# Optimization experiments

Hardware: AMD Instinct MI355X
Metric: run time of the kernel (lower is better)

## Reference

```python
import jax, jax.numpy as jnp
import numpy as np

WS = 8        # window_size
NH = 16       # num_heads

def setup_inputs() -> dict:
    key = jax.random.key(0)
    k1, k2, k3, k4 = jax.random.split(key, 4)
    B, N, C = 16, 4096, 512
    x = jax.random.normal(k1, (B, N, C), dtype=jnp.float32)
    w_qkv = jax.random.normal(k2, (3 * C, C), dtype=jnp.float32) * 0.02
    w_proj = jax.random.normal(k3, (C, C), dtype=jnp.float32) * 0.02
    b_proj = jax.random.normal(k4, (C,), dtype=jnp.float32) * 0.02
    return {"x": x, "w_qkv": w_qkv, "w_proj": w_proj, "b_proj": b_proj}

def reference(x, w_qkv, w_proj, b_proj):
    B, N, C = x.shape
    H = W = int(N ** 0.5)
    ws, nh = WS, NH
    hd = C // nh
    scale = hd ** (-0.5)
    winH, winW = H // ws, W // ws

    # --- window partition, faithfully replicating torch unfold+view semantics ---
    # unfold(1).unfold(2).contiguous() memory layout: (B, winH, winW, C, ws_h, ws_w)
    xw = x.reshape(B, winH, ws, winW, ws, C)
    xw = jnp.transpose(xw, (0, 1, 3, 5, 2, 4))  # (B,winH,winW,C,ws,ws) contiguous order
    # torch .view(B,winH,winW,ws,ws,C): pure reshape of that layout (scrambles C/spatial)
    xw = xw.reshape(B, winH, winW, ws, ws, C)
    xw = jnp.transpose(xw, (0, 1, 2, 4, 3, 5)).reshape(-1, ws * ws, C)  # (nW, ws*ws, C)

    # --- qkv projection and per-window attention ---
    qkv = (xw @ w_qkv.T).reshape(-1, ws * ws, 3, nh, hd)
    qkv = jnp.transpose(qkv, (2, 0, 3, 1, 4))  # (3, nW, nh, ws*ws, hd)
    q, k, v = qkv[0], qkv[1], qkv[2]
    attn = jnp.einsum('whid,whjd->whij', q, k) * scale
    attn = jax.nn.softmax(attn, axis=-1)
    o = jnp.einsum('whij,whjd->whid', attn, v)          # (nW, nh, ws*ws, hd)
    o = jnp.transpose(o, (0, 2, 1, 3)).reshape(-1, ws * ws, C)

    o = o @ w_proj.T + b_proj

    # --- window merge (standard permute, as in torch code) ---
    o = o.reshape(B, winH, winW, ws, ws, C)
    o = jnp.transpose(o, (0, 1, 3, 2, 4, 5)).reshape(B, H, W, C)
    return o.reshape(B, N, C)
```

## Files before the change

### kernel.cpp

```cpp
#include <hip/hip_runtime.h>


typedef short s16x8 __attribute__((ext_vector_type(8)));
typedef float f32x4 __attribute__((ext_vector_type(4)));

union V8 { uint4 u4; uint2 u2[2]; s16x8 h; ushort s[8]; uint u[4]; };

__device__ __forceinline__ ushort f2b(float f) {
    union { float f; uint u; } v; v.f = f;
    return (ushort)((v.u + 0x7fffu + ((v.u >> 16) & 1u)) >> 16);
}
__device__ __forceinline__ void cvt8(const float* __restrict__ p, V8& d) {
    union { float4 f; uint u[4]; } a, b;
    a.f = *(const float4*)p;  b.f = *(const float4*)(p + 4);
    d.u[0] = __builtin_amdgcn_perm(a.u[1], a.u[0], 0x07060302u);
    d.u[1] = __builtin_amdgcn_perm(a.u[3], a.u[2], 0x07060302u);
    d.u[2] = __builtin_amdgcn_perm(b.u[1], b.u[0], 0x07060302u);
    d.u[3] = __builtin_amdgcn_perm(b.u[3], b.u[2], 0x07060302u);
}
__device__ __forceinline__ f32x4 mfma16(s16x8 a, s16x8 b, f32x4 c) {
    return __builtin_amdgcn_mfma_f32_16x16x32_bf16(a, b, c, 0, 0, 0);
}
__device__ __forceinline__ uint2 pack4(float a, float b, float c, float d) {
    uint2 r;
    r.x = (uint)f2b(a) | ((uint)f2b(b) << 16);
    r.y = (uint)f2b(c) | ((uint)f2b(d) << 16);
    return r;
}

__global__ __launch_bounds__(256)
void pack_w(const float* __restrict__ wqkv, const float* __restrict__ wproj,
            ushort* __restrict__ dst)
{
    const int gid = blockIdx.x * 256 + threadIdx.x;
    const int o = gid << 3;
    const int colw = (o >> 3) & 15, quad = (o >> 7) & 3, kk = (o >> 9) & 15;
    const int tile = o >> 13;
    const float* src;
    if (o < 786432) {
        const int mat = tile >> 5, nt = tile & 31;
        src = wqkv + (size_t)(mat * 512 + nt * 16 + colw) * 512 + (kk << 5) + (quad << 3);
    } else {
        const int nt = tile - 96;
        src = wproj + (size_t)(nt * 16 + colw) * 512 + (kk << 5) + (quad << 3);
    }
    float4 a = *(const float4*)src, b = *(const float4*)(src + 4);
    V8 v;
    v.s[0] = f2b(a.x); v.s[1] = f2b(a.y); v.s[2] = f2b(a.z); v.s[3] = f2b(a.w);
    v.s[4] = f2b(b.x); v.s[5] = f2b(b.y); v.s[6] = f2b(b.z); v.s[7] = f2b(b.w);
    *(uint4*)(dst + o) = v.u4;
}

template<bool PK>
__global__ __launch_bounds__(1024, 4)
void win_fused(const float* __restrict__ x, const void* __restrict__ Wq,
               const void* __restrict__ Wp, const float* __restrict__ bproj,
               float* __restrict__ out)
{
    __shared__ __align__(16) ushort xw[32768];
    __shared__ __align__(16) ushort scr[32768];

    char* const sb = (char*)scr;
    const int tid  = threadIdx.x;
    const int lane = tid & 63;
    const int wave = tid >> 6;
    const int col  = lane & 15, quad = lane >> 4;
    const int win  = blockIdx.x;
    const int bb = win >> 6, wh = (win >> 3) & 7, ww = win & 7;
    const size_t xbase = (size_t)(bb * 4096) * 512;

    {
        const int m8 = lane;
        const int u8 = wave & 7;
        const int dh = wave >> 3;
        const int t  = ((m8 & 7) << 3) | (m8 >> 3);
        const int ch0 = m8 << 3;
        const float* gp = x + xbase
            + (size_t)(wh * 512 + u8 * 64 + ww * 8 + dh * 4) * 512 + ch0;
        V8 L[4];
        #pragma unroll
        for (int i = 0; i < 4; ++i) cvt8(gp + i * 512, L[i]);
        #pragma unroll
        for (int e = 0; e < 8; ++e) {
            union { uint2 u; ushort s[4]; } Wv;
            #pragma unroll
            for (int i = 0; i < 4; ++i) Wv.s[i] = L[i].s[e];
            const int c8 = (e << 3) | u8;
            *(uint2*)(&xw[(t << 9) + ((c8 ^ (t & 7)) << 3) + (dh << 2)]) = Wv.u;
        }
    }
    __syncthreads();

    const int hhg = wave >> 2;
    const int mh  = (wave >> 1) & 1;
    const int nhf = wave & 1;
    const int tw  = wave & 3;

    f32x4 pacc[4][2];
    #pragma unroll
    for (int mt = 0; mt < 4; ++mt) {
        pacc[mt][0] = (f32x4){0.f, 0.f, 0.f, 0.f};
        pacc[mt][1] = (f32x4){0.f, 0.f, 0.f, 0.f};
    }

    for (int p = 0; p < 4; ++p) {
        const int h = (p << 2) | hhg;

        f32x4 c00 = {0.f,0.f,0.f,0.f}, c01 = {0.f,0.f,0.f,0.f}, c02 = {0.f,0.f,0.f,0.f};
        f32x4 c10 = {0.f,0.f,0.f,0.f}, c11 = {0.f,0.f,0.f,0.f}, c12 = {0.f,0.f,0.f,0.f};
        size_t wb0 = 0, wb1 = 0, wb2 = 0;
        const float *f0 = nullptr, *f1 = nullptr, *f2 = nullptr;
        if constexpr (PK) {
            if (nhf == 0) { wb0 = (size_t)(2*h)   * 8192; wb1 = (size_t)(2*h+1)  * 8192;
                            wb2 = (size_t)(32+2*h)* 8192; }
            else          { wb0 = (size_t)(32+2*h+1)*8192; wb1 = (size_t)(64+2*h)*8192;
                            wb2 = (size_t)(64+2*h+1)*8192; }
        } else {
            const float* W = (const float*)Wq;
            if (nhf == 0) {
                f0 = W + (size_t)(h*32 + col) * 512;
                f1 = W + (size_t)(h*32 + 16 + col) * 512;
                f2 = W + (size_t)(512 + h*32 + col) * 512;
            } else {
                f0 = W + (size_t)(512 + h*32 + 16 + col) * 512;
                f1 = W + (size_t)(1024 + h*32 + col) * 512;
                f2 = W + (size_t)(1024 + h*32 + 16 + col) * 512;
            }
        }
        #pragma unroll 2
        for (int kk = 0; kk < 16; ++kk) {
            const int c8 = (kk << 2) | quad;
            V8 a0, a1;
            { const int t = mh*32 + col;      a0.u4 = *(const uint4*)(&xw[(t << 9) + ((c8 ^ (t & 7)) << 3)]); }
            { const int t = mh*32 + 16 + col; a1.u4 = *(const uint4*)(&xw[(t << 9) + ((c8 ^ (t & 7)) << 3)]); }
            V8 b0, b1, b2;
            if constexpr (PK) {
                const ushort* W = (const ushort*)Wq;
                const int lo = (kk << 9) + (lane << 3);
                b0.u4 = *(const uint4*)(&W[wb0 + lo]);
                b1.u4 = *(const uint4*)(&W[wb1 + lo]);
                b2.u4 = *(const uint4*)(&W[wb2 + lo]);
            } else {
                cvt8(f0 + (kk << 5) + (quad << 3), b0);
                cvt8(f1 + (kk << 5) + (quad << 3), b1);
                cvt8(f2 + (kk << 5) + (quad << 3), b2);
            }
            c00 = mfma16(a0.h, b0.h, c00);
            c01 = mfma16(a0.h, b1.h, c01);
            c02 = mfma16(a0.h, b2.h, c02);
            c10 = mfma16(a1.h, b0.h, c10);
            c11 = mfma16(a1.h, b1.h, c11);
            c12 = mfma16(a1.h, b2.h, c12);
        }

        {
            const int hb = hhg * 12288;
            #pragma unroll
            for (int mt = 0; mt < 2; ++mt) {
                const int tokb = mh*32 + mt*16 + (quad << 2);
                const f32x4& d0 = mt ? c10 : c00;
                const f32x4& d1 = mt ? c11 : c01;
                const f32x4& d2 = mt ? c12 : c02;
                if (nhf == 0) {
                    #pragma unroll
                    for (int r = 0; r < 4; ++r) {
                        const int rowb = hb + ((tokb + r) << 6);
                        *(ushort*)(sb + rowb + ((col*2)      ^ (quad << 4))) = f2b(d0[r]);
                        *(ushort*)(sb + rowb + ((32 + col*2) ^ (quad << 4))) = f2b(d1[r]);
                        *(ushort*)(sb + 4096 + rowb + ((col*2) ^ (quad << 4))) = f2b(d2[r]);
                    }
                } else {
                    #pragma unroll
                    for (int r = 0; r < 4; ++r) {
                        const int rowb = hb + ((tokb + r) << 6);
                        *(ushort*)(sb + 4096 + rowb + ((32 + col*2) ^ (quad << 4))) = f2b(d0[r]);
                    }
                    const int tsw = (tokb * 2) ^ ((col & 7) << 4);
                    *(uint2*)(sb + hb + 8192 + col * 128 + tsw) =
                        pack4(d1[0], d1[1], d1[2], d1[3]);
                    *(uint2*)(sb + hb + 8192 + (16 + col) * 128 + tsw) =
                        pack4(d2[0], d2[1], d2[2], d2[3]);
                }
            }
        }
        __syncthreads();

        const int ab = hhg * 12288;
        const int sr = ((col >> 2) & 3) << 4;
        V8 kf0, kf1, kf2, kf3, qf;
        kf0.u4 = *(const uint4*)(sb + ab + 4096 + ((0*16 + col) << 6) + ((quad << 4) ^ sr));
        kf1.u4 = *(const uint4*)(sb + ab + 4096 + ((1*16 + col) << 6) + ((quad << 4) ^ sr));
        kf2.u4 = *(const uint4*)(sb + ab + 4096 + ((2*16 + col) << 6) + ((quad << 4) ^ sr));
        kf3.u4 = *(const uint4*)(sb + ab + 4096 + ((3*16 + col) << 6) + ((quad << 4) ^ sr));
        qf.u4  = *(const uint4*)(sb + ab + (((tw << 4) + col) << 6) + ((quad << 4) ^ sr));
        f32x4 ST[4];
        ST[0] = mfma16(kf0.h, qf.h, (f32x4){0.f,0.f,0.f,0.f});
        ST[1] = mfma16(kf1.h, qf.h, (f32x4){0.f,0.f,0.f,0.f});
        ST[2] = mfma16(kf2.h, qf.h, (f32x4){0.f,0.f,0.f,0.f});
        ST[3] = mfma16(kf3.h, qf.h, (f32x4){0.f,0.f,0.f,0.f});

        const float smul = 0.17677669529663689f * 1.4426950408889634f;
        float m0 = ST[0][0];
        #pragma unroll
        for (int a = 0; a < 4; ++a)
            #pragma unroll
            for (int r = 0; r < 4; ++r) m0 = fmaxf(m0, ST[a][r]);
        m0 = fmaxf(m0, __shfl_xor(m0, 16));
        m0 = fmaxf(m0, __shfl_xor(m0, 32));
        float s0 = 0.f;
        #pragma unroll
        for (int a = 0; a < 4; ++a)
            #pragma unroll
            for (int r = 0; r < 4; ++r) {
                const float pv = exp2f((ST[a][r] - m0) * smul);
                ST[a][r] = pv; s0 += pv;
            }
        s0 += __shfl_xor(s0, 16);
        s0 += __shfl_xor(s0, 32);
        const float inv = 1.0f / s0;

        const uint2 pk0 = pack4(ST[0][0], ST[0][1], ST[0][2], ST[0][3]);
        const uint2 pk1 = pack4(ST[1][0], ST[1][1], ST[1][2], ST[1][3]);
        const uint2 pk2 = pack4(ST[2][0], ST[2][1], ST[2][2], ST[2][3]);
        const uint2 pk3 = pack4(ST[3][0], ST[3][1], ST[3][2], ST[3][3]);
        const int srcA = ((quad & 1) << 5) + col;
        const int srcB = srcA + 16;
        const bool hi = quad >= 2;
        f32x4 OT0 = {0.f,0.f,0.f,0.f}, OT1 = {0.f,0.f,0.f,0.f};
        const int vsw = (col & 7) << 4;
        {
            const uint a0x = __shfl((int)pk0.x, srcA), a0y = __shfl((int)pk0.y, srcA);
            const uint b0x = __shfl((int)pk0.x, srcB), b0y = __shfl((int)pk0.y, srcB);
            const uint a1x = __shfl((int)pk1.x, srcA), a1y = __shfl((int)pk1.y, srcA);
            const uint b1x = __shfl((int)pk1.x, srcB), b1y = __shfl((int)pk1.y, srcB);
            V8 pf;
            pf.u[0] = hi ? a1x : a0x;  pf.u[1] = hi ? a1y : a0y;
            pf.u[2] = hi ? b1x : b0x;  pf.u[3] = hi ? b1y : b0y;
            V8 vf0, vf1;
            vf0.u4 = *(const uint4*)(sb + ab + 8192 + ((0*16 + col) << 7) + (((quad << 4)) ^ vsw));
            vf1.u4 = *(const uint4*)(sb + ab + 8192 + ((16 + col) << 7)   + (((quad << 4)) ^ vsw));
            OT0 = mfma16(vf0.h, pf.h, OT0);
            OT1 = mfma16(vf1.h, pf.h, OT1);
        }
        {
            const uint a0x = __shfl((int)pk2.x, srcA), a0y = __shfl((int)pk2.y, srcA);
            const uint b0x = __shfl((int)pk2.x, srcB), b0y = __shfl((int)pk2.y, srcB);
            const uint a1x = __shfl((int)pk3.x, srcA), a1y = __shfl((int)pk3.y, srcA);
            const uint b1x = __shfl((int)pk3.x, srcB), b1y = __shfl((int)pk3.y, srcB);
            V8 pf;
            pf.u[0] = hi ? a1x : a0x;  pf.u[1] = hi ? a1y : a0y;
            pf.u[2] = hi ? b1x : b0x;  pf.u[3] = hi ? b1y : b0y;
            V8 vf0, vf1;
            vf0.u4 = *(const uint4*)(sb + ab + 8192 + ((0*16 + col) << 7) + ((64 + (quad << 4)) ^ vsw));
            vf1.u4 = *(const uint4*)(sb + ab + 8192 + ((16 + col) << 7)   + ((64 + (quad << 4)) ^ vsw));
            OT0 = mfma16(vf0.h, pf.h, OT0);
            OT1 = mfma16(vf1.h, pf.h, OT1);
        }

        {
            const int rowb = 49152 + (((tw << 4) + col) << 8);
            const int osw = (col & 3) << 5;
            const int ch2a = hhg*64 + (quad << 3);
            *(uint2*)(sb + rowb + (ch2a ^ osw)) =
                pack4(OT0[0]*inv, OT0[1]*inv, OT0[2]*inv, OT0[3]*inv);
            *(uint2*)(sb + rowb + ((ch2a + 32) ^ osw)) =
                pack4(OT1[0]*inv, OT1[1]*inv, OT1[2]*inv, OT1[3]*inv);
        }
        __syncthreads();

        #pragma unroll 2
        for (int kkl = 0; kkl < 4; ++kkl) {
            const int kkg = (p << 2) | kkl;
            V8 a0, a1, a2, a3;
            const int cb = ((kkl << 6) + (quad << 4));
            const int osw = (col & 3) << 5;
            a0.u4 = *(const uint4*)(sb + 49152 + ((0*16 + col) << 8) + (cb ^ osw));
            a1.u4 = *(const uint4*)(sb + 49152 + ((1*16 + col) << 8) + (cb ^ osw));
            a2.u4 = *(const uint4*)(sb + 49152 + ((2*16 + col) << 8) + (cb ^ osw));
            a3.u4 = *(const uint4*)(sb + 49152 + ((3*16 + col) << 8) + (cb ^ osw));
            #pragma unroll
            for (int nt = 0; nt < 2; ++nt) {
                s16x8 b;
                if constexpr (PK) {
                    const ushort* W = (const ushort*)Wp;
                    V8 v; v.u4 = *(const uint4*)(&W[(size_t)(((wave*2 + nt)*16) + kkg) * 512
                                                    + (lane << 3)]);
                    b = v.h;
                } else {
                    const float* W = (const float*)Wp;
                    V8 v; cvt8(W + (size_t)(wave*32 + nt*16 + col) * 512
                                 + (kkg << 5) + (quad << 3), v);
                    b = v.h;
                }
                pacc[0][nt] = mfma16(a0.h, b, pacc[0][nt]);
                pacc[1][nt] = mfma16(a1.h, b, pacc[1][nt]);
                pacc[2][nt] = mfma16(a2.h, b, pacc[2][nt]);
                pacc[3][nt] = mfma16(a3.h, b, pacc[3][nt]);
            }
        }
    }

    const size_t wbase = (size_t)(bb * 4096 + wh * 512 + ww * 8) * 512;
    const float bv0 = bproj[wave*32 + col];
    const float bv1 = bproj[wave*32 + 16 + col];
    #pragma unroll
    for (int mt = 0; mt < 4; ++mt)
        #pragma unroll
        for (int r = 0; r < 4; ++r) {
            const int t = (mt << 4) + (quad << 2) + r;
            float* op = out + wbase + (size_t)(((t >> 3) << 6) + (t & 7)) * 512
                        + wave*32;
            op[col]      = pacc[mt][0][r] + bv0;
            op[16 + col] = pacc[mt][1][r] + bv1;
        }
}

extern "C" void kernel_launch(void* const* d_in, const int* in_sizes, int n_in,
                              void* d_out, int out_size, void* d_ws, size_t ws_size,
                              hipStream_t stream) {
    const float* x     = (const float*)d_in[0];
    const float* wqkv  = (const float*)d_in[1];
    const float* wproj = (const float*)d_in[2];
    const float* bproj = (const float*)d_in[3];
    float* out = (float*)d_out;
    (void)in_sizes; (void)n_in; (void)out_size;

    if (ws_size >= 2097152) {
        ushort* wpk = (ushort*)d_ws;
        pack_w<<<dim3(512), dim3(256), 0, stream>>>(wqkv, wproj, wpk);
        win_fused<true><<<dim3(1024), dim3(1024), 0, stream>>>(
            x, wpk, wpk + 786432, bproj, out);
    } else {
        win_fused<false><<<dim3(1024), dim3(1024), 0, stream>>>(
            x, wqkv, wproj, bproj, out);
    }
}
```

Before: 428.4 us.

## Process eight heads per pass with full-token QKV tiles per wave

Each wave now computes QKV for one head across all 64 tokens, so 8 heads are handled per pass instead of 4. This halves the outer head-group loop from 4 passes to 2 and each weight fragment load is reused across four M tiles instead of two, which cuts redundant weight traffic. Shared memory is enlarged to one 160KB buffer so the scratch area can hold eight heads. Attention then handles two query tiles per wave, and the projection runs over eight K-steps per pass. In exchange there are more accumulator registers and more LDS, which may limit occupancy.

```diff
diff --git a/kernel.cpp b/kernel.cpp
--- a/kernel.cpp
+++ b/kernel.cpp
@@ -57,10 +57,10 @@
                const void* __restrict__ Wp, const float* __restrict__ bproj,
                float* __restrict__ out)
 {
-    __shared__ __align__(16) ushort xw[32768];
-    __shared__ __align__(16) ushort scr[32768];
-
-    char* const sb = (char*)scr;
+    __shared__ __align__(16) ushort sm[81920];
+    ushort* const xw = sm;
+    char* const sb = (char*)(sm + 32768);
+
     const int tid  = threadIdx.x;
     const int lane = tid & 63;
     const int wave = tid >> 6;
@@ -91,10 +91,8 @@
     }
     __syncthreads();
 
-    const int hhg = wave >> 2;
-    const int mh  = (wave >> 1) & 1;
-    const int nhf = wave & 1;
-    const int tw  = wave & 3;
+    const int hh  = wave >> 1;
+    const int tri = wave & 1;
 
     f32x4 pacc[4][2];
     #pragma unroll
@@ -102,22 +100,26 @@
         pacc[mt][0] = (f32x4){0.f, 0.f, 0.f, 0.f};
         pacc[mt][1] = (f32x4){0.f, 0.f, 0.f, 0.f};
     }
-
-    for (int p = 0; p < 4; ++p) {
-        const int h = (p << 2) | hhg;
-
-        f32x4 c00 = {0.f,0.f,0.f,0.f}, c01 = {0.f,0.f,0.f,0.f}, c02 = {0.f,0.f,0.f,0.f};
-        f32x4 c10 = {0.f,0.f,0.f,0.f}, c11 = {0.f,0.f,0.f,0.f}, c12 = {0.f,0.f,0.f,0.f};
+    const float smul = 0.17677669529663689f * 1.4426950408889634f;
+
+    for (int p = 0; p < 2; ++p) {
+        const int h = (p << 3) | hh;
+
+        f32x4 c[4][3];
+        #pragma unroll
+        for (int mt = 0; mt < 4; ++mt)
+            #pragma unroll
+            for (int nt = 0; nt < 3; ++nt) c[mt][nt] = (f32x4){0.f, 0.f, 0.f, 0.f};
         size_t wb0 = 0, wb1 = 0, wb2 = 0;
         const float *f0 = nullptr, *f1 = nullptr, *f2 = nullptr;
         if constexpr (PK) {
-            if (nhf == 0) { wb0 = (size_t)(2*h)   * 8192; wb1 = (size_t)(2*h+1)  * 8192;
-                            wb2 = (size_t)(32+2*h)* 8192; }
-            else          { wb0 = (size_t)(32+2*h+1)*8192; wb1 = (size_t)(64+2*h)*8192;
-                            wb2 = (size_t)(64+2*h+1)*8192; }
+            if (tri == 0) { wb0 = (size_t)(2*h)     * 8192; wb1 = (size_t)(2*h+1)  * 8192;
+                            wb2 = (size_t)(32+2*h)  * 8192; }
+            else          { wb0 = (size_t)(32+2*h+1)* 8192; wb1 = (size_t)(64+2*h) * 8192;
+                            wb2 = (size_t)(64+2*h+1)* 8192; }
         } else {
             const float* W = (const float*)Wq;
-            if (nhf == 0) {
+            if (tri == 0) {
                 f0 = W + (size_t)(h*32 + col) * 512;
                 f1 = W + (size_t)(h*32 + 16 + col) * 512;
                 f2 = W + (size_t)(512 + h*32 + col) * 512;
@@ -130,9 +132,6 @@
         #pragma unroll 2
         for (int kk = 0; kk < 16; ++kk) {
             const int c8 = (kk << 2) | quad;
-            V8 a0, a1;
-            { const int t = mh*32 + col;      a0.u4 = *(const uint4*)(&xw[(t << 9) + ((c8 ^ (t & 7)) << 3)]); }
-            { const int t = mh*32 + 16 + col; a1.u4 = *(const uint4*)(&xw[(t << 9) + ((c8 ^ (t & 7)) << 3)]); }
             V8 b0, b1, b2;
             if constexpr (PK) {
                 const ushort* W = (const ushort*)Wq;
@@ -145,157 +144,169 @@
                 cvt8(f1 + (kk << 5) + (quad << 3), b1);
                 cvt8(f2 + (kk << 5) + (quad << 3), b2);
             }
-            c00 = mfma16(a0.h, b0.h, c00);
-            c01 = mfma16(a0.h, b1.h, c01);
-            c02 = mfma16(a0.h, b2.h, c02);
-            c10 = mfma16(a1.h, b0.h, c10);
-            c11 = mfma16(a1.h, b1.h, c11);
-            c12 = mfma16(a1.h, b2.h, c12);
-        }
+            #pragma unroll
+            for (int mt = 0; mt < 4; ++mt) {
+                const int t = (mt << 4) + col;
+                V8 a; a.u4 = *(const uint4*)(&xw[(t << 9) + ((c8 ^ (t & 7)) << 3)]);
+                c[mt][0] = mfma16(a.h, b0.h, c[mt][0]);
+                c[mt][1] = mfma16(a.h, b1.h, c[mt][1]);
+                c[mt][2] = mfma16(a.h, b2.h, c[mt][2]);
+            }
+        }
+
+        if (p) __syncthreads();
 
         {
-            const int hb = hhg * 12288;
-            #pragma unroll
-            for (int mt = 0; mt < 2; ++mt) {
-                const int tokb = mh*32 + mt*16 + (quad << 2);
-                const f32x4& d0 = mt ? c10 : c00;
-                const f32x4& d1 = mt ? c11 : c01;
-                const f32x4& d2 = mt ? c12 : c02;
-                if (nhf == 0) {
+            const int hb = hh * 12288;
+            if (tri == 0) {
+                #pragma unroll
+                for (int mt = 0; mt < 4; ++mt)
                     #pragma unroll
                     for (int r = 0; r < 4; ++r) {
-                        const int rowb = hb + ((tokb + r) << 6);
-                        *(ushort*)(sb + rowb + ((col*2)      ^ (quad << 4))) = f2b(d0[r]);
-                        *(ushort*)(sb + rowb + ((32 + col*2) ^ (quad << 4))) = f2b(d1[r]);
-                        *(ushort*)(sb + 4096 + rowb + ((col*2) ^ (quad << 4))) = f2b(d2[r]);
+                        const int tok  = (mt << 4) + (quad << 2) + r;
+                        const int rowb = hb + (tok << 6);
+                        const int s    = quad << 4;
+                        *(ushort*)(sb + rowb + ((col*2)        ^ s)) = f2b(c[mt][0][r]);
+                        *(ushort*)(sb + rowb + ((32 + col*2)   ^ s)) = f2b(c[mt][1][r]);
+                        *(ushort*)(sb + 4096 + rowb + ((col*2) ^ s)) = f2b(c[mt][2][r]);
                     }
-                } else {
+            } else {
+                #pragma unroll
+                for (int mt = 0; mt < 4; ++mt) {
                     #pragma unroll
                     for (int r = 0; r < 4; ++r) {
-                        const int rowb = hb + ((tokb + r) << 6);
-                        *(ushort*)(sb + 4096 + rowb + ((32 + col*2) ^ (quad << 4))) = f2b(d0[r]);
+                        const int tok = (mt << 4) + (quad << 2) + r;
+                        *(ushort*)(sb + hb + 4096 + (tok << 6)
+                                   + ((32 + col*2) ^ (quad << 4))) = f2b(c[mt][0][r]);
                     }
-                    const int tsw = (tokb * 2) ^ ((col & 7) << 4);
-                    *(uint2*)(sb + hb + 8192 + col * 128 + tsw) =
-                        pack4(d1[0], d1[1], d1[2], d1[3]);
+                    const int tok0 = (mt << 4) + (quad << 2);
+                    const int tsw  = (tok0 * 2) ^ ((col & 7) << 4);
+                    *(uint2*)(sb + hb + 8192 + col * 128        + tsw) =
+                        pack4(c[mt][1][0], c[mt][1][1], c[mt][1][2], c[mt][1][3]);
                     *(uint2*)(sb + hb + 8192 + (16 + col) * 128 + tsw) =
-                        pack4(d2[0], d2[1], d2[2], d2[3]);
+                        pack4(c[mt][2][0], c[mt][2][1], c[mt][2][2], c[mt][2][3]);
                 }
             }
         }
         __syncthreads();
 
-        const int ab = hhg * 12288;
-        const int sr = ((col >> 2) & 3) << 4;
-        V8 kf0, kf1, kf2, kf3, qf;
-        kf0.u4 = *(const uint4*)(sb + ab + 4096 + ((0*16 + col) << 6) + ((quad << 4) ^ sr));
-        kf1.u4 = *(const uint4*)(sb + ab + 4096 + ((1*16 + col) << 6) + ((quad << 4) ^ sr));
-        kf2.u4 = *(const uint4*)(sb + ab + 4096 + ((2*16 + col) << 6) + ((quad << 4) ^ sr));
-        kf3.u4 = *(const uint4*)(sb + ab + 4096 + ((3*16 + col) << 6) + ((quad << 4) ^ sr));
-        qf.u4  = *(const uint4*)(sb + ab + (((tw << 4) + col) << 6) + ((quad << 4) ^ sr));
-        f32x4 ST[4];
-        ST[0] = mfma16(kf0.h, qf.h, (f32x4){0.f,0.f,0.f,0.f});
-        ST[1] = mfma16(kf1.h, qf.h, (f32x4){0.f,0.f,0.f,0.f});
-        ST[2] = mfma16(kf2.h, qf.h, (f32x4){0.f,0.f,0.f,0.f});
-        ST[3] = mfma16(kf3.h, qf.h, (f32x4){0.f,0.f,0.f,0.f});
-
-        const float smul = 0.17677669529663689f * 1.4426950408889634f;
-        float m0 = ST[0][0];
-        #pragma unroll
-        for (int a = 0; a < 4; ++a)
-            #pragma unroll
-            for (int r = 0; r < 4; ++r) m0 = fmaxf(m0, ST[a][r]);
-        m0 = fmaxf(m0, __shfl_xor(m0, 16));
-        m0 = fmaxf(m0, __shfl_xor(m0, 32));
-        float s0 = 0.f;
-        #pragma unroll
-        for (int a = 0; a < 4; ++a)
-            #pragma unroll
-            for (int r = 0; r < 4; ++r) {
-                const float pv = exp2f((ST[a][r] - m0) * smul);
-                ST[a][r] = pv; s0 += pv;
-            }
-        s0 += __shfl_xor(s0, 16);
-        s0 += __shfl_xor(s0, 32);
-        const float inv = 1.0f / s0;
-
-        const uint2 pk0 = pack4(ST[0][0], ST[0][1], ST[0][2], ST[0][3]);
-        const uint2 pk1 = pack4(ST[1][0], ST[1][1], ST[1][2], ST[1][3]);
-        const uint2 pk2 = pack4(ST[2][0], ST[2][1], ST[2][2], ST[2][3]);
-        const uint2 pk3 = pack4(ST[3][0], ST[3][1], ST[3][2], ST[3][3]);
-        const int srcA = ((quad & 1) << 5) + col;
-        const int srcB = srcA + 16;
-        const bool hi = quad >= 2;
-        f32x4 OT0 = {0.f,0.f,0.f,0.f}, OT1 = {0.f,0.f,0.f,0.f};
-        const int vsw = (col & 7) << 4;
         {
-            const uint a0x = __shfl((int)pk0.x, srcA), a0y = __shfl((int)pk0.y, srcA);
-            const uint b0x = __shfl((int)pk0.x, srcB), b0y = __shfl((int)pk0.y, srcB);
-            const uint a1x = __shfl((int)pk1.x, srcA), a1y = __shfl((int)pk1.y, srcA);
-            const uint b1x = __shfl((int)pk1.x, srcB), b1y = __shfl((int)pk1.y, srcB);
-            V8 pf;
-            pf.u[0] = hi ? a1x : a0x;  pf.u[1] = hi ? a1y : a0y;
-            pf.u[2] = hi ? b1x : b0x;  pf.u[3] = hi ? b1y : b0y;
-            V8 vf0, vf1;
-            vf0.u4 = *(const uint4*)(sb + ab + 8192 + ((0*16 + col) << 7) + (((quad << 4)) ^ vsw));
-            vf1.u4 = *(const uint4*)(sb + ab + 8192 + ((16 + col) << 7)   + (((quad << 4)) ^ vsw));
-            OT0 = mfma16(vf0.h, pf.h, OT0);
-            OT1 = mfma16(vf1.h, pf.h, OT1);
-        }
-        {
-            const uint a0x = __shfl((int)pk2.x, srcA), a0y = __shfl((int)pk2.y, srcA);
-            const uint b0x = __shfl((int)pk2.x, srcB), b0y = __shfl((int)pk2.y, srcB);
-            const uint a1x = __shfl((int)pk3.x, srcA), a1y = __shfl((int)pk3.y, srcA);
-            const uint b1x = __shfl((int)pk3.x, srcB), b1y = __shfl((int)pk3.y, srcB);
-            V8 pf;
-            pf.u[0] = hi ? a1x : a0x;  pf.u[1] = hi ? a1y : a0y;
-            pf.u[2] = hi ? b1x : b0x;  pf.u[3] = hi ? b1y : b0y;
-            V8 vf0, vf1;
-            vf0.u4 = *(const uint4*)(sb + ab + 8192 + ((0*16 + col) << 7) + ((64 + (quad << 4)) ^ vsw));
-            vf1.u4 = *(const uint4*)(sb + ab + 8192 + ((16 + col) << 7)   + ((64 + (quad << 4)) ^ vsw));
-            OT0 = mfma16(vf0.h, pf.h, OT0);
-            OT1 = mfma16(vf1.h, pf.h, OT1);
-        }
-
-        {
-            const int rowb = 49152 + (((tw << 4) + col) << 8);
-            const int osw = (col & 3) << 5;
-            const int ch2a = hhg*64 + (quad << 3);
-            *(uint2*)(sb + rowb + (ch2a ^ osw)) =
-                pack4(OT0[0]*inv, OT0[1]*inv, OT0[2]*inv, OT0[3]*inv);
-            *(uint2*)(sb + rowb + ((ch2a + 32) ^ osw)) =
-                pack4(OT1[0]*inv, OT1[1]*inv, OT1[2]*inv, OT1[3]*inv);
+            const int ab = hh * 12288;
+            const int sr = ((col >> 2) & 3) << 4;
+            s16x8 kf[4];
+            #pragma unroll
+            for (int kt = 0; kt < 4; ++kt) {
+                V8 v; v.u4 = *(const uint4*)(sb + ab + 4096
+                              + (((kt << 4) + col) << 6) + ((quad << 4) ^ sr));
+                kf[kt] = v.h;
+            }
+            float inv[2]; uint2 pk[4][2];
+            #pragma unroll
+            for (int qt = 0; qt < 2; ++qt) {
+                V8 qf; qf.u4 = *(const uint4*)(sb + ab
+                               + ((((tri*2 + qt) << 4) + col) << 6) + ((quad << 4) ^ sr));
+                f32x4 ST[4];
+                #pragma unroll
+                for (int kt = 0; kt < 4; ++kt)
+                    ST[kt] = mfma16(kf[kt], qf.h, (f32x4){0.f,0.f,0.f,0.f});
+                float m0 = ST[0][0];
+                #pragma unroll
+                for (int kt = 0; kt < 4; ++kt)
+                    #pragma unroll
+                    for (int r = 0; r < 4; ++r) m0 = fmaxf(m0, ST[kt][r]);
+                m0 = fmaxf(m0, __shfl_xor(m0, 16));
+                m0 = fmaxf(m0, __shfl_xor(m0, 32));
+                float s0 = 0.f;
+                #pragma unroll
+                for (int kt = 0; kt < 4; ++kt)
+                    #pragma unroll
+                    for (int r = 0; r < 4; ++r) {
+                        const float pv = exp2f((ST[kt][r] - m0) * smul);
+                        ST[kt][r] = pv; s0 += pv;
+                    }
+                s0 += __shfl_xor(s0, 16);
+                s0 += __shfl_xor(s0, 32);
+                inv[qt] = 1.0f / s0;
+                #pragma unroll
+                for (int kt = 0; kt < 4; ++kt)
+                    pk[kt][qt] = pack4(ST[kt][0], ST[kt][1], ST[kt][2], ST[kt][3]);
+            }
+
+            f32x4 OT[2][2];
+            #pragma unroll
+            for (int dt = 0; dt < 2; ++dt) {
+                OT[dt][0] = (f32x4){0.f,0.f,0.f,0.f};
+                OT[dt][1] = (f32x4){0.f,0.f,0.f,0.f};
+            }
+            const int srcA = ((quad & 1) << 5) + col;
+            const int srcB = srcA + 16;
+            const bool hi = quad >= 2;
+            const int vsw = (col & 7) << 4;
+            #pragma unroll
+            for (int kh = 0; kh < 2; ++kh) {
+                s16x8 pf[2];
+                #pragma unroll
+                for (int qt = 0; qt < 2; ++qt) {
+                    const uint2 pkA = pk[kh*2][qt], pkB = pk[kh*2+1][qt];
+                    const uint a0x = __shfl((int)pkA.x, srcA), a0y = __shfl((int)pkA.y, srcA);
+                    const uint b0x = __shfl((int)pkA.x, srcB), b0y = __shfl((int)pkA.y, srcB);
+                    const uint a1x = __shfl((int)pkB.x, srcA), a1y = __shfl((int)pkB.y, srcA);
+                    const uint b1x = __shfl((int)pkB.x, srcB), b1y = __shfl((int)pkB.y, srcB);
+                    V8 t;
+                    t.u[0] = hi ? a1x : a0x;  t.u[1] = hi ? a1y : a0y;
+                    t.u[2] = hi ? b1x : b0x;  t.u[3] = hi ? b1y : b0y;
+                    pf[qt] = t.h;
+                }
+                #pragma unroll
+                for (int dt = 0; dt < 2; ++dt) {
+                    V8 vf; vf.u4 = *(const uint4*)(sb + ab + 8192
+                                   + (((dt << 4) + col) << 7)
+                                   + (((kh << 6) + (quad << 4)) ^ vsw));
+                    OT[dt][0] = mfma16(vf.h, pf[0], OT[dt][0]);
+                    OT[dt][1] = mfma16(vf.h, pf[1], OT[dt][1]);
+                }
+            }
+            __syncthreads();
+
+            #pragma unroll
+            for (int dt = 0; dt < 2; ++dt)
+                #pragma unroll
+                for (int qt = 0; qt < 2; ++qt) {
+                    const int tok   = ((tri*2 + qt) << 4) + col;
+                    const int choff = (hh << 6) + (dt << 5) + (quad << 3);
+                    *(uint2*)(sb + (tok << 9) + (choff ^ ((col & 7) << 6))) =
+                        pack4(OT[dt][qt][0]*inv[qt], OT[dt][qt][1]*inv[qt],
+                              OT[dt][qt][2]*inv[qt], OT[dt][qt][3]*inv[qt]);
+                }
         }
         __syncthreads();
 
         #pragma unroll 2
-        for (int kkl = 0; kkl < 4; ++kkl) {
-            const int kkg = (p << 2) | kkl;
-            V8 a0, a1, a2, a3;
-            const int cb = ((kkl << 6) + (quad << 4));
-            const int osw = (col & 3) << 5;
-            a0.u4 = *(const uint4*)(sb + 49152 + ((0*16 + col) << 8) + (cb ^ osw));
-            a1.u4 = *(const uint4*)(sb + 49152 + ((1*16 + col) << 8) + (cb ^ osw));
-            a2.u4 = *(const uint4*)(sb + 49152 + ((2*16 + col) << 8) + (cb ^ osw));
-            a3.u4 = *(const uint4*)(sb + 49152 + ((3*16 + col) << 8) + (cb ^ osw));
+        for (int kkl = 0; kkl < 8; ++kkl) {
+            const int kkg = (p << 3) | kkl;
+            V8 a[4];
+            const int osw = (col & 7) << 6;
+            #pragma unroll
+            for (int mt = 0; mt < 4; ++mt)
+                a[mt].u4 = *(const uint4*)(sb + (((mt << 4) + col) << 9)
+                            + (((kkl << 6) + (quad << 4)) ^ osw));
             #pragma unroll
             for (int nt = 0; nt < 2; ++nt) {
                 s16x8 b;
                 if constexpr (PK) {
                     const ushort* W = (const ushort*)Wp;
-                    V8 v; v.u4 = *(const uint4*)(&W[(size_t)(((wave*2 + nt)*16) + kkg) * 512
+                    V8 v; v.u4 = *(const uint4*)(&W[(size_t)(((wave*2 + nt) << 4) + kkg) * 512
                                                     + (lane << 3)]);
                     b = v.h;
                 } else {
                     const float* W = (const float*)Wp;
-                    V8 v; cvt8(W + (size_t)(wave*32 + nt*16 + col) * 512
+                    V8 v; cvt8(W + (size_t)(wave*32 + (nt << 4) + col) * 512
                                  + (kkg << 5) + (quad << 3), v);
                     b = v.h;
                 }
-                pacc[0][nt] = mfma16(a0.h, b, pacc[0][nt]);
-                pacc[1][nt] = mfma16(a1.h, b, pacc[1][nt]);
-                pacc[2][nt] = mfma16(a2.h, b, pacc[2][nt]);
-                pacc[3][nt] = mfma16(a3.h, b, pacc[3][nt]);
+                #pragma unroll
+                for (int mt = 0; mt < 4; ++mt)
+                    pacc[mt][nt] = mfma16(a[mt].h, b, pacc[mt][nt]);
             }
         }
     }
```

Result: no change. 431.3 us (+0.7%).
